# Kernel optimization log

Hardware: AMD Instinct MI355X
Metric: run time of the kernel (lower is better)

## Reference

```python
import jax, jax.numpy as jnp
import numpy as np


def setup_inputs() -> dict:
    key = jax.random.key(0)
    k1, k2 = jax.random.split(key)
    B, T, F = 8, 1000, 257
    m = jax.random.normal(k1, (B, 27, T, F), dtype=jnp.float32)
    x = jax.random.normal(k2, (B, F, T, 2), dtype=jnp.float32)
    return {"m": m, "x": x}


def reference(m, x):
    # m: (B, 27, T, F) real; x: (B, F, T, 2) real (re/im stacked)
    B, _, T, F = m.shape
    SQ3_2 = float(np.sqrt(3.0) / 2.0)
    v = jnp.array([1.0 + 0.0j, -0.5 + 1j * SQ3_2, -0.5 - 1j * SQ3_2],
                  dtype=jnp.complex64)  # complex basis, shape (3,)
    # (b, 3, 9, t, f) -> contract basis axis -> complex (b, 9, t, f)
    mr = m.reshape(B, 3, 9, T, F).astype(jnp.complex64)
    H = jnp.einsum('r,brctf->bctf', v, mr)
    M = H.reshape(B, 3, 3, T, F)  # per-pixel 3x3 complex mask

    # complex spectrogram (B, T, F); original permutes (B,F,T,2)->(B,2,T,F)
    xc = (x[..., 0] + 1j * x[..., 1]).transpose(0, 2, 1)
    # ZeroPad2d([1,1,2,0]) on (T,F): top=2 (causal time), left=right=1 (freq)
    xp = jnp.pad(xc, ((0, 0), (2, 0), (1, 1)))

    # Fused stencil: accumulate 3x3 complex MAC without materializing unfold
    x_enh = jnp.zeros((B, T, F), dtype=jnp.complex64)
    for mm in range(3):
        for nn in range(3):
            x_enh = x_enh + M[:, mm, nn] * xp[:, mm:mm + T, nn:nn + F]

    # (B,T,F) complex -> (B,T,F,2) -> (B,F,T,2)
    out = jnp.stack([x_enh.real, x_enh.imag], axis=-1).transpose(0, 2, 1, 3)
    return out
```

## Files before the change

### kernel.cpp

```cpp
#include <hip/hip_runtime.h>

#define B_  8
#define T_  1000
#define F_  257
#define TP  (T_ + 2)
#define FP  (F_ + 2)
#define SQ3_2 0.8660254037844386f

__global__ __launch_bounds__(256)
void transpose_pad(const float2* __restrict__ x, float2* __restrict__ xp) {
    __shared__ float2 tile[32][33];
    const int b   = blockIdx.z;
    const int tp0 = blockIdx.x * 32;
    const int fp0 = blockIdx.y * 32;
    const int tx  = threadIdx.x;
    const int ty  = threadIdx.y;

    #pragma unroll
    for (int k = 0; k < 4; ++k) {
        const int fl = ty + k * 8;
        const int t  = tp0 + tx - 2;
        const int f  = fp0 + fl - 1;
        float2 v = make_float2(0.f, 0.f);
        if (t >= 0 && t < T_ && f >= 0 && f < F_)
            v = x[(size_t)(b * F_ + f) * T_ + t];
        tile[fl][tx] = v;
    }
    __syncthreads();

    #pragma unroll
    for (int k = 0; k < 4; ++k) {
        const int tp = tp0 + ty + k * 8;
        const int fp = fp0 + tx;
        if (tp < TP && fp < FP)
            xp[((size_t)b * TP + tp) * FP + fp] = tile[tx][ty + k * 8];
    }
}

__global__ __launch_bounds__(512)
void ccm_main(const float* __restrict__ m, const float2* __restrict__ xp,
              float2* __restrict__ out) {
    __shared__ float2 stage[8][66];

    const int b   = blockIdx.z;
    const int f0  = blockIdx.x * 64;
    const int t0  = blockIdx.y * 8;
    const int tid = threadIdx.x;
    const int lf  = tid & 63;
    const int lt  = tid >> 6;
    const int f   = f0 + lf;
    const int t   = t0 + lt;

    float accr = 0.f, acci = 0.f;

    if (f < F_) {
        const float2* xpb = xp + (size_t)b * TP * FP;
        float2 tap[3][3];
        #pragma unroll
        for (int mm = 0; mm < 3; ++mm)
            #pragma unroll
            for (int nn = 0; nn < 3; ++nn)
                tap[mm][nn] = xpb[(size_t)(t + mm) * FP + (f + nn)];

        const float* mb = m + ((size_t)b * 27 * T_ + t) * F_ + f;
        #pragma unroll
        for (int c = 0; c < 9; ++c) {
            const float m0 = mb[(size_t)(c)      * (T_ * F_)];
            const float m1 = mb[(size_t)(c + 9)  * (T_ * F_)];
            const float m2 = mb[(size_t)(c + 18) * (T_ * F_)];
            const float hr = m0 - 0.5f * (m1 + m2);
            const float hi = SQ3_2 * (m1 - m2);
            const float2 xv = tap[c / 3][c % 3];
            accr = fmaf(hr, xv.x, accr);
            accr = fmaf(-hi, xv.y, accr);
            acci = fmaf(hr, xv.y, acci);
            acci = fmaf(hi, xv.x, acci);
        }
    }

    stage[lt][lf] = make_float2(accr, acci);
    __syncthreads();

    const int wf = tid >> 3;
    const int wt = tid & 7;
    if (f0 + wf < F_)
        out[(size_t)(b * F_ + f0 + wf) * T_ + (t0 + wt)] = stage[wt][wf];
}

extern "C" void kernel_launch(void* const* d_in, const int* in_sizes, int n_in,
                              void* d_out, int out_size, void* d_ws, size_t ws_size,
                              hipStream_t stream) {
    const float*  m = (const float*)d_in[0];
    const float2* x = (const float2*)d_in[1];
    float2* out = (float2*)d_out;
    float2* xp  = (float2*)d_ws;

    dim3 tb(32, 8);
    dim3 tg((TP + 31) / 32, (FP + 31) / 32, B_);
    transpose_pad<<<tg, tb, 0, stream>>>(x, xp);

    dim3 mb(512);
    dim3 mg((F_ + 63) / 64, T_ / 8, B_);
    ccm_main<<<mg, mb, 0, stream>>>(m, xp, out);
}
```

Baseline: 324.5 us.

## Fuse transpose-pad into main kernel via shared-memory halo tile

Drops the separate transpose/pad kernel and its padded workspace buffer. Each block now loads its 10x66 halo tile of x straight from the (B,F,T) layout into shared memory, zero-filling at the edges, and reads the nine stencil taps from LDS. This removes one launch and a full write plus re-read of the padded spectrogram. In exchange the global loads of x are strided (only 10 contiguous t values per f), and a sync plus LDS traffic are added.

```diff
diff --git a/kernel.cpp b/kernel.cpp
--- a/kernel.cpp
+++ b/kernel.cpp
@@ -3,43 +3,12 @@
 #define B_  8
 #define T_  1000
 #define F_  257
-#define TP  (T_ + 2)
-#define FP  (F_ + 2)
 #define SQ3_2 0.8660254037844386f
 
-__global__ __launch_bounds__(256)
-void transpose_pad(const float2* __restrict__ x, float2* __restrict__ xp) {
-    __shared__ float2 tile[32][33];
-    const int b   = blockIdx.z;
-    const int tp0 = blockIdx.x * 32;
-    const int fp0 = blockIdx.y * 32;
-    const int tx  = threadIdx.x;
-    const int ty  = threadIdx.y;
-
-    #pragma unroll
-    for (int k = 0; k < 4; ++k) {
-        const int fl = ty + k * 8;
-        const int t  = tp0 + tx - 2;
-        const int f  = fp0 + fl - 1;
-        float2 v = make_float2(0.f, 0.f);
-        if (t >= 0 && t < T_ && f >= 0 && f < F_)
-            v = x[(size_t)(b * F_ + f) * T_ + t];
-        tile[fl][tx] = v;
-    }
-    __syncthreads();
-
-    #pragma unroll
-    for (int k = 0; k < 4; ++k) {
-        const int tp = tp0 + ty + k * 8;
-        const int fp = fp0 + tx;
-        if (tp < TP && fp < FP)
-            xp[((size_t)b * TP + tp) * FP + fp] = tile[tx][ty + k * 8];
-    }
-}
-
 __global__ __launch_bounds__(512)
-void ccm_main(const float* __restrict__ m, const float2* __restrict__ xp,
-              float2* __restrict__ out) {
+void ccm_fused(const float* __restrict__ m, const float2* __restrict__ x,
+               float2* __restrict__ out) {
+    __shared__ float2 xls[10 * 66];
     __shared__ float2 stage[8][66];
 
     const int b   = blockIdx.z;
@@ -51,17 +20,26 @@
     const int f   = f0 + lf;
     const int t   = t0 + lt;
 
+    const float2* xb = x + (size_t)b * F_ * T_;
+    #pragma unroll
+    for (int pass = 0; pass < 2; ++pass) {
+        const int idx = tid + pass * 512;
+        if (idx < 660) {
+            const int j = idx / 10;
+            const int r = idx - j * 10;
+            const int tt = t0 + r - 2;
+            const int ff = f0 + j - 1;
+            float2 v = make_float2(0.f, 0.f);
+            if (tt >= 0 && tt < T_ && ff >= 0 && ff < F_)
+                v = xb[(size_t)ff * T_ + tt];
+            xls[r * 66 + j] = v;
+        }
+    }
+    __syncthreads();
+
     float accr = 0.f, acci = 0.f;
 
     if (f < F_) {
-        const float2* xpb = xp + (size_t)b * TP * FP;
-        float2 tap[3][3];
-        #pragma unroll
-        for (int mm = 0; mm < 3; ++mm)
-            #pragma unroll
-            for (int nn = 0; nn < 3; ++nn)
-                tap[mm][nn] = xpb[(size_t)(t + mm) * FP + (f + nn)];
-
         const float* mb = m + ((size_t)b * 27 * T_ + t) * F_ + f;
         #pragma unroll
         for (int c = 0; c < 9; ++c) {
@@ -70,7 +48,7 @@
             const float m2 = mb[(size_t)(c + 18) * (T_ * F_)];
             const float hr = m0 - 0.5f * (m1 + m2);
             const float hi = SQ3_2 * (m1 - m2);
-            const float2 xv = tap[c / 3][c % 3];
+            const float2 xv = xls[(lt + c / 3) * 66 + (lf + c % 3)];
             accr = fmaf(hr, xv.x, accr);
             accr = fmaf(-hi, xv.y, accr);
             acci = fmaf(hr, xv.y, acci);
@@ -93,13 +71,8 @@
     const float*  m = (const float*)d_in[0];
     const float2* x = (const float2*)d_in[1];
     float2* out = (float2*)d_out;
-    float2* xp  = (float2*)d_ws;
-
-    dim3 tb(32, 8);
-    dim3 tg((TP + 31) / 32, (FP + 31) / 32, B_);
-    transpose_pad<<<tg, tb, 0, stream>>>(x, xp);
 
     dim3 mb(512);
     dim3 mg((F_ + 63) / 64, T_ / 8, B_);
-    ccm_main<<<mg, mb, 0, stream>>>(m, xp, out);
+    ccm_fused<<<mg, mb, 0, stream>>>(m, x, out);
 }
```

Result: no change. 321.3 us (-1.0%).
